# Kernel tuning notes

Measured on AMD Instinct MI355X. Metric: run time of the kernel, lower is better.

Reference implementation:

```python
import jax, jax.numpy as jnp
import numpy as np

D_MODEL = 2048
N_HEADS = 16
N_KV = 4
D_HEAD = D_MODEL // N_HEADS  # 128
N_REP = N_HEADS // N_KV      # 4
ROPE_BASE = 1000000.0


def _rope_tables(T, d_head, dtype):
    # inv_freq = (1/base)^(2i/d) for i in [0, d/2)
    i = jnp.arange(d_head // 2, dtype=jnp.float32)
    inv_freq = (1.0 / ROPE_BASE) ** (2.0 * i / d_head)
    theta = jnp.arange(T, dtype=jnp.float32)[:, None] * inv_freq[None, :]  # [T, d/2]
    theta = jnp.concatenate([theta, theta], axis=-1)                        # [T, d]
    return jnp.sin(theta).astype(dtype), jnp.cos(theta).astype(dtype)


def _apply_rope(x, sin, cos):
    # x: [B, h, T, d]; sin/cos: [T, d]
    x1, x2 = jnp.split(x, 2, axis=-1)
    rot = jnp.concatenate([-x2, x1], axis=-1)
    return cos[None, None] * x + sin[None, None] * rot


def setup_inputs() -> dict:
    key = jax.random.key(0)
    ks = jax.random.split(key, 9)
    B, T = 2, 2048
    s_in = 1.0 / np.sqrt(D_MODEL)
    return {
        "x": jax.random.normal(ks[0], (B, T, D_MODEL), jnp.float32),
        "wq": jax.random.normal(ks[1], (D_MODEL, N_HEADS * D_HEAD), jnp.float32) * s_in,
        "bq": jax.random.normal(ks[2], (N_HEADS * D_HEAD,), jnp.float32) * 0.02,
        "wk": jax.random.normal(ks[3], (D_MODEL, N_KV * D_HEAD), jnp.float32) * s_in,
        "bk": jax.random.normal(ks[4], (N_KV * D_HEAD,), jnp.float32) * 0.02,
        "wv": jax.random.normal(ks[5], (D_MODEL, N_KV * D_HEAD), jnp.float32) * s_in,
        "bv": jax.random.normal(ks[6], (N_KV * D_HEAD,), jnp.float32) * 0.02,
        "wo": jax.random.normal(ks[7], (D_MODEL, D_MODEL), jnp.float32) * s_in,
    }


def reference(x, wq, bq, wk, bk, wv, bv, wo):
    B, T, C = x.shape
    sin, cos = _rope_tables(T, D_HEAD, x.dtype)

    q = (x @ wq + bq).reshape(B, T, N_HEADS, D_HEAD).transpose(0, 2, 1, 3)  # [B,H,T,d]
    k = (x @ wk + bk).reshape(B, T, N_KV, D_HEAD).transpose(0, 2, 1, 3)     # [B,KV,T,d]
    v = (x @ wv + bv).reshape(B, T, N_KV, D_HEAD).transpose(0, 2, 1, 3)     # [B,KV,T,d]

    q = _apply_rope(q, sin, cos)
    k = _apply_rope(k, sin, cos)

    # GQA: group query heads as [B, KV, rep, T, d] to broadcast against k/v
    qg = q.reshape(B, N_KV, N_REP, T, D_HEAD)
    scale = 1.0 / jnp.sqrt(jnp.asarray(D_HEAD, x.dtype))
    scores = jnp.einsum('bkrqd,bksd->bkrqs', qg, k) * scale  # [B,KV,rep,T,S]

    causal = jnp.tril(jnp.ones((T, T), dtype=bool))
    neg = jnp.asarray(jnp.finfo(x.dtype).min, x.dtype)
    scores = jnp.where(causal[None, None, None], scores, neg)
    p = jax.nn.softmax(scores, axis=-1)

    out = jnp.einsum('bkrqs,bksd->bkrqd', p, v)               # [B,KV,rep,T,d]
    out = out.reshape(B, N_HEADS, T, D_HEAD).transpose(0, 2, 1, 3).reshape(B, T, C)
    return out @ wo, k, v
```

## Files before the change

kernel.cpp:

```cpp
#include <hip/hip_runtime.h>
#include <hip/hip_bf16.h>
#include <math.h>

#define BB 2
#define TT 2048
#define DMODEL 2048
#define NH 16
#define NKV 4
#define DH 128
#define NQKV 3072
#define MM (BB*TT)

typedef unsigned short u16;
typedef unsigned int u32;

typedef __bf16 bf16x8 __attribute__((ext_vector_type(8)));
typedef __bf16 bf16x4 __attribute__((ext_vector_type(4)));
typedef short short4v __attribute__((ext_vector_type(4)));
typedef float f32x4 __attribute__((ext_vector_type(4)));

__device__ __forceinline__ u16 f2b(float f) {
  union { float f; u32 u; } v; v.f = f;
  u32 r = v.u + 0x7fffu + ((v.u >> 16) & 1u);
  return (u16)(r >> 16);
}
__device__ __forceinline__ float b2f(u16 h) {
  union { u32 u; float f; } v; v.u = ((u32)h) << 16;
  return v.f;
}
__device__ __forceinline__ u32 pack2bf(float x, float y) {
  union { float f; u32 u; } a, b; a.f = x; b.f = y;
  return ((a.u + 0x8000u) >> 16) | ((b.u + 0x8000u) & 0xffff0000u);
}

__device__ __forceinline__ void gload16(const void* g, void* l) {
  __builtin_amdgcn_global_load_lds(
      (const __attribute__((address_space(1))) unsigned int*)g,
      (__attribute__((address_space(3))) unsigned int*)l, 16, 0, 0);
}

__device__ __forceinline__ float fast_exp2(float x) {
#if __has_builtin(__builtin_amdgcn_exp2f)
  return __builtin_amdgcn_exp2f(x);
#else
  return __expf(x * 0.6931471805599453f);
#endif
}

__device__ __forceinline__ f32x4 mfma16(bf16x4 a, bf16x4 b, f32x4 c) {
#if __has_builtin(__builtin_amdgcn_mfma_f32_16x16x16bf16_1k)
  union { bf16x4 b; short4v s; } ua, ub;
  ua.b = a; ub.b = b;
  return __builtin_amdgcn_mfma_f32_16x16x16bf16_1k(ua.s, ub.s, c, 0, 0, 0);
#elif __has_builtin(__builtin_amdgcn_mfma_f32_16x16x16_bf16)
  return __builtin_amdgcn_mfma_f32_16x16x16_bf16(a, b, c, 0, 0, 0);
#else
  asm volatile("v_mfma_f32_16x16x16_bf16 %0, %1, %2, %0"
               : "+v"(c) : "v"(a), "v"(b));
  return c;
#endif
}

__global__ void cvt_x_kernel(const float* __restrict__ x, u16* __restrict__ xb, int n4) {
  int i = blockIdx.x * 256 + threadIdx.x;
  if (i < n4) {
    float4 v = ((const float4*)x)[i];
    u32 lo = (u32)f2b(v.x) | ((u32)f2b(v.y) << 16);
    u32 hi = (u32)f2b(v.z) | ((u32)f2b(v.w) << 16);
    uint2 r; r.x = lo; r.y = hi;
    ((uint2*)xb)[i] = r;
  }
}

__global__ void rope_table_kernel(float2* __restrict__ tab) {
  int i = blockIdx.x * 256 + threadIdx.x;
  int t = i >> 6, d = i & 63;
  float inv = exp2f(-(float)d * 0.31143075889569023f);
  float th = (float)t * inv;
  float2 cs; cs.x = cosf(th); cs.y = sinf(th);
  tab[i] = cs;
}

__global__ void transpose_cvt_kernel(const float* __restrict__ src, u16* __restrict__ dst,
                                     int srcCols, int dstRowOff) {
  __shared__ u16 t[64][65];
  int c0 = blockIdx.x * 64, r0 = blockIdx.y * 64;
  int tid = threadIdx.x;
  for (int i = tid; i < 4096; i += 256) {
    int r = i >> 6, c = i & 63;
    t[r][c] = f2b(src[(size_t)(r0 + r) * srcCols + c0 + c]);
  }
  __syncthreads();
  for (int i = tid; i < 4096; i += 256) {
    int n = i >> 6, k = i & 63;
    dst[(size_t)(dstRowOff + c0 + n) * 2048 + r0 + k] = t[k][n];
  }
}

__global__ __launch_bounds__(256, 3) void gemm_qkv_kernel(
    const u16* __restrict__ A, const u16* __restrict__ Bt,
    const float* __restrict__ bq, const float* __restrict__ bk,
    const float* __restrict__ bv, const float2* __restrict__ rtab,
    u16* __restrict__ qb, u16* __restrict__ kb, u16* __restrict__ vt,
    float* __restrict__ outK, float* __restrict__ outV) {
  __shared__ __align__(16) u16 sm[16384];
  const int K = DMODEL;
  const int tid  = threadIdx.x;
  const int lane = tid & 63;
  const int wave = tid >> 6;
  const int quad = lane >> 4;
  const int l16  = lane & 15;
  const int m0 = blockIdx.y * 128;
  const int n0 = blockIdx.x * 128;
  const int nh = blockIdx.x;
  const int wrow = (wave >> 1) * 64;
  const int wcol = (wave & 1) * 64;

  f32x4 acc[4][4];
  const f32x4 zero = {0.f, 0.f, 0.f, 0.f};
#pragma unroll
  for (int i = 0; i < 4; i++)
#pragma unroll
    for (int j = 0; j < 4; j++) acc[i][j] = zero;

  const int srow = tid >> 2;
  const int scol = (tid & 3) * 8;
  const u16* ga = A  + (size_t)(m0 + srow) * K + scol;
  const u16* gb = Bt + (size_t)(n0 + srow) * K + scol;

  gload16(ga,                  &sm[tid * 8]);
  gload16(ga + (size_t)64 * K, &sm[2048 + tid * 8]);
  gload16(gb,                  &sm[4096 + tid * 8]);
  gload16(gb + (size_t)64 * K, &sm[6144 + tid * 8]);

  for (int k0 = 0; k0 < K; k0 += 32) {
    const int p = (k0 >> 5) & 1;
    const int kn = (k0 + 32 == K) ? 0 : k0 + 32;
    u16* nb = &sm[(p ^ 1) * 8192];
    gload16(ga + kn,                  nb + tid * 8);
    gload16(ga + kn + (size_t)64 * K, nb + 2048 + tid * 8);
    gload16(gb + kn,                  nb + 4096 + tid * 8);
    gload16(gb + kn + (size_t)64 * K, nb + 6144 + tid * 8);
    asm volatile("s_waitcnt vmcnt(4)\n\ts_barrier" ::: "memory");
    const u16* cb = &sm[p * 8192];
    bf16x8 af[4], bf[4];
#pragma unroll
    for (int mi = 0; mi < 4; mi++)
      af[mi] = *(const bf16x8*)&cb[(wrow + mi * 16 + l16) * 32 + quad * 8];
#pragma unroll
    for (int ni = 0; ni < 4; ni++)
      bf[ni] = *(const bf16x8*)&cb[4096 + (wcol + ni * 16 + l16) * 32 + quad * 8];
    asm volatile("s_waitcnt lgkmcnt(0)\n\ts_barrier" ::: "memory");
#pragma unroll
    for (int mi = 0; mi < 4; mi++)
#pragma unroll
      for (int ni = 0; ni < 4; ni++)
        acc[mi][ni] = __builtin_amdgcn_mfma_f32_16x16x32_bf16(af[mi], bf[ni], acc[mi][ni], 0, 0, 0);
  }

  asm volatile("s_waitcnt vmcnt(0)\n\ts_barrier" ::: "memory");

#pragma unroll
  for (int ni = 0; ni < 4; ni++) {
    int col = wcol + ni * 16 + l16;
    int gcol = n0 + col;
    float bval = (nh < 16) ? bq[gcol] : ((nh < 20) ? bk[gcol - 2048] : bv[gcol - 2560]);
#pragma unroll
    for (int mi = 0; mi < 4; mi++) {
#pragma unroll
      for (int r = 0; r < 4; r++) {
        int row = wrow + mi * 16 + quad * 4 + r;
        sm[row * 128 + col] = f2b(acc[mi][ni][r] + bval);
      }
    }
  }
  __syncthreads();

  const int bidx = m0 >> 11;
  const int trow0 = m0 & 2047;

  if (nh < 20) {
    const int isQ = (nh < 16);
    const int hh = isQ ? nh : (nh - 16);
#pragma unroll
    for (int it = 0; it < 4; it++) {
      int id = tid + it * 256;
      int row = id >> 3, oc = id & 7;
      int t = trow0 + row;
      int rl = t & 63, ttile = t >> 6;
      uint4 lo = *(const uint4*)&sm[row * 128 + oc * 8];
      uint4 hi = *(const uint4*)&sm[row * 128 + 64 + oc * 8];
      const u16* plo = (const u16*)&lo;
      const u16* phi = (const u16*)&hi;
      u16 y1[8], y2[8];
      float f1[8], f2v[8];
#pragma unroll
      for (int j = 0; j < 8; j++) {
        float2 cs = rtab[(t << 6) + oc * 8 + j];
        float x1 = b2f(plo[j]), x2 = b2f(phi[j]);
        f1[j]  = cs.x * x1 - cs.y * x2;
        f2v[j] = cs.x * x2 + cs.y * x1;
        y1[j] = f2b(f1[j]);
        y2[j] = f2b(f2v[j]);
      }
      if (isQ) {
        size_t tb = ((size_t)(bidx * NH + hh) * 32 + ttile) * 8192;
        *(uint4*)&qb[tb + (size_t)((oc)     * 64 + rl) * 8] = *(const uint4*)y1;
        *(uint4*)&qb[tb + (size_t)((oc + 8) * 64 + rl) * 8] = *(const uint4*)y2;
      } else {
        size_t tb = ((size_t)(bidx * NKV + hh) * 32 + ttile) * 8192;
        *(uint4*)&kb[tb + (size_t)((oc)     * 64 + rl) * 8] = *(const uint4*)y1;
        *(uint4*)&kb[tb + (size_t)((oc + 8) * 64 + rl) * 8] = *(const uint4*)y2;
        size_t base = ((size_t)(bidx * NKV + hh) * TT + t) * DH + oc * 8;
        *(float4*)&outK[base]          = *(const float4*)&f1[0];
        *(float4*)&outK[base + 4]      = *(const float4*)&f1[4];
        *(float4*)&outK[base + 64]     = *(const float4*)&f2v[0];
        *(float4*)&outK[base + 64 + 4] = *(const float4*)&f2v[4];
      }
    }
  } else {
    const int kvh = nh - 20;
#pragma unroll
    for (int it = 0; it < 8; it++) {
      int id = tid + it * 256;
      int row = id >> 4, oc = id & 15;
      uint4 v = *(const uint4*)&sm[row * 128 + oc * 8];
      const u16* pv = (const u16*)&v;
      float f[8];
#pragma unroll
      for (int j = 0; j < 8; j++) f[j] = b2f(pv[j]);
      size_t base = ((size_t)(bidx * NKV + kvh) * TT + trow0 + row) * DH + oc * 8;
      *(float4*)&outV[base]     = *(const float4*)&f[0];
      *(float4*)&outV[base + 4] = *(const float4*)&f[4];
    }
#pragma unroll
    for (int it = 0; it < 8; it++) {
      int id = tid + it * 256;
      int tile = id >> 10, rem = id & 1023;
      int chunk = rem >> 7, dl = rem & 127;
      int m = chunk >> 2, qd = chunk & 3;
      u16 tmp[8];
#pragma unroll
      for (int e = 0; e < 8; e++) {
        int srw = (2 * m + (e >> 2)) * 16 + qd * 4 + (e & 3);
        tmp[e] = sm[(tile * 64 + srw) * 128 + dl];
      }
      int tt = (trow0 >> 6) + tile;
      size_t tilebase = ((size_t)(bidx * NKV + kvh) * 32 + tt) * 8192;
      *(uint4*)&vt[tilebase + (size_t)(chunk * 128 + dl) * 8] = *(const uint4*)tmp;
    }
  }
}

__global__ __launch_bounds__(256, 3) void gemm_out_kernel(
    const u16* __restrict__ A, const u16* __restrict__ Bt,
    float* __restrict__ Cout, int M, int N, int K) {
  __shared__ __align__(16) u16 sm[16384];
  const int tid  = threadIdx.x;
  const int lane = tid & 63;
  const int wave = tid >> 6;
  const int quad = lane >> 4;
  const int l16  = lane & 15;
  const int m0 = blockIdx.y * 128;
  const int n0 = blockIdx.x * 128;
  const int wrow = (wave >> 1) * 64;
  const int wcol = (wave & 1) * 64;

  f32x4 acc[4][4];
  const f32x4 zero = {0.f, 0.f, 0.f, 0.f};
#pragma unroll
  for (int i = 0; i < 4; i++)
#pragma unroll
    for (int j = 0; j < 4; j++) acc[i][j] = zero;

  const int srow = tid >> 2;
  const int scol = (tid & 3) * 8;
  const u16* ga = A  + (size_t)(m0 + srow) * K + scol;
  const u16* gb = Bt + (size_t)(n0 + srow) * K + scol;

  gload16(ga,                  &sm[tid * 8]);
  gload16(ga + (size_t)64 * K, &sm[2048 + tid * 8]);
  gload16(gb,                  &sm[4096 + tid * 8]);
  gload16(gb + (size_t)64 * K, &sm[6144 + tid * 8]);

  for (int k0 = 0; k0 < K; k0 += 32) {
    const int p = (k0 >> 5) & 1;
    const int kn = (k0 + 32 == K) ? 0 : k0 + 32;
    u16* nb = &sm[(p ^ 1) * 8192];
    gload16(ga + kn,                  nb + tid * 8);
    gload16(ga + kn + (size_t)64 * K, nb + 2048 + tid * 8);
    gload16(gb + kn,                  nb + 4096 + tid * 8);
    gload16(gb + kn + (size_t)64 * K, nb + 6144 + tid * 8);
    asm volatile("s_waitcnt vmcnt(4)\n\ts_barrier" ::: "memory");
    const u16* cb = &sm[p * 8192];
    bf16x8 af[4], bf[4];
#pragma unroll
    for (int mi = 0; mi < 4; mi++)
      af[mi] = *(const bf16x8*)&cb[(wrow + mi * 16 + l16) * 32 + quad * 8];
#pragma unroll
    for (int ni = 0; ni < 4; ni++)
      bf[ni] = *(const bf16x8*)&cb[4096 + (wcol + ni * 16 + l16) * 32 + quad * 8];
    asm volatile("s_waitcnt lgkmcnt(0)\n\ts_barrier" ::: "memory");
#pragma unroll
    for (int mi = 0; mi < 4; mi++)
#pragma unroll
      for (int ni = 0; ni < 4; ni++)
        acc[mi][ni] = __builtin_amdgcn_mfma_f32_16x16x32_bf16(af[mi], bf[ni], acc[mi][ni], 0, 0, 0);
  }
  asm volatile("s_waitcnt vmcnt(0)" ::: "memory");

#pragma unroll
  for (int ni = 0; ni < 4; ni++) {
    int gcol = n0 + wcol + ni * 16 + l16;
#pragma unroll
    for (int mi = 0; mi < 4; mi++) {
#pragma unroll
      for (int r = 0; r < 4; r++) {
        int grow = m0 + wrow + mi * 16 + quad * 4 + r;
        Cout[(size_t)grow * N + gcol] = acc[mi][ni][r];
      }
    }
  }
}

__global__ __launch_bounds__(256, 2) void attn_kernel(
    const u16* __restrict__ Qt, const u16* __restrict__ Kt,
    const u16* __restrict__ Vt, u16* __restrict__ Ob) {
  __shared__ __align__(16) u16 sm[24576];
  u16* vbuf = sm + 16384;

  const int bh = blockIdx.y;
  const int b = bh >> 4, h = bh & 15, kv = h >> 2;
  const int tid = threadIdx.x;
  const int lane = tid & 63;
  const int wave = tid >> 6;
  const int quad = lane >> 4;
  const int l16 = lane & 15;

  const u16* qbase = Qt + (size_t)(b * NH + h) * 32 * 8192;
  const u16* kbase = Kt + (size_t)(b * NKV + kv) * 32 * 8192;
  const u16* vbase = Vt + (size_t)(b * NKV + kv) * 32 * 8192;

  const f32x4 zero = {0.f, 0.f, 0.f, 0.f};
  const float SC2 = 0.08838834764831845f * 1.4426950408889634f;
  const float NEGINF = -__builtin_inff();

  int par = 0;

#pragma unroll
  for (int p = 0; p < 4; p++)
    gload16(kbase + p * 2048 + tid * 8, sm + p * 2048 + tid * 8);

  for (int half = 0; half < 2; ++half) {
    const int qt = half ? (31 - (int)blockIdx.x) : (int)blockIdx.x;
    const int q0 = qt * 64;
    const u16* qtile = qbase + (size_t)qt * 8192;
    const int qrel = wave * 16 + l16;

    bf16x8 qf[4];
#pragma unroll
    for (int kc = 0; kc < 4; kc++)
      qf[kc] = *(const bf16x8*)&qtile[(size_t)((kc * 4 + quad) * 64 + qrel) * 8];

    float mrow = NEGINF, lrow = 0.f;
    f32x4 o[8];
#pragma unroll
    for (int d = 0; d < 8; d++) o[d] = zero;

    for (int kt = 0; kt <= qt; ++kt) {
      u16* kb_c = sm + par * 8192;
      u16* kb_n = sm + (par ^ 1) * 8192;
      const int ktn = (kt < qt) ? kt + 1 : 0;
      const u16* vsrc = vbase + (size_t)kt * 8192;
      const u16* knxt = kbase + (size_t)ktn * 8192;
#pragma unroll
      for (int p = 0; p < 4; p++)
        gload16(vsrc + p * 2048 + tid * 8, vbuf + p * 2048 + tid * 8);
#pragma unroll
      for (int p = 0; p < 4; p++)
        gload16(knxt + p * 2048 + tid * 8, kb_n + p * 2048 + tid * 8);
      asm volatile("s_waitcnt vmcnt(8)\n\ts_barrier" ::: "memory");

      f32x4 sv[4];
#pragma unroll
      for (int mt = 0; mt < 4; mt++) sv[mt] = zero;
#pragma unroll
      for (int kc = 0; kc < 4; kc++) {
#pragma unroll
        for (int mt = 0; mt < 4; mt++) {
          bf16x8 kf = *(const bf16x8*)&kb_c[(size_t)((kc * 4 + quad) * 64 + mt * 16 + l16) * 8];
          sv[mt] = __builtin_amdgcn_mfma_f32_16x16x32_bf16(kf, qf[kc], sv[mt], 0, 0, 0);
        }
      }

      if (kt == qt) {
#pragma unroll
        for (int mt = 0; mt < 4; mt++)
#pragma unroll
          for (int r = 0; r < 4; r++) {
            int srel = mt * 16 + quad * 4 + r;
            if (srel > qrel) sv[mt][r] = NEGINF;
          }
      }
      float mraw = NEGINF;
#pragma unroll
      for (int mt = 0; mt < 4; mt++)
#pragma unroll
        for (int r = 0; r < 4; r++) mraw = fmaxf(mraw, sv[mt][r]);
      mraw = fmaxf(mraw, __shfl_xor(mraw, 16));
      mraw = fmaxf(mraw, __shfl_xor(mraw, 32));

      float mnew = fmaxf(mrow, mraw);
      float alpha = fast_exp2((mrow - mnew) * SC2);
      mrow = mnew;
      float msc = mnew * SC2;
      float lsum = 0.f;
#pragma unroll
      for (int mt = 0; mt < 4; mt++) {
#pragma unroll
        for (int r = 0; r < 4; r++) {
          float p = fast_exp2(__builtin_fmaf(sv[mt][r], SC2, -msc));
          sv[mt][r] = p;
          lsum += p;
        }
      }
      lrow = lrow * alpha + lsum;
      bf16x4 pb[4];
#pragma unroll
      for (int mt = 0; mt < 4; mt++) {
        union { u32 u[2]; bf16x4 v; } pu;
        pu.u[0] = pack2bf(sv[mt][0], sv[mt][1]);
        pu.u[1] = pack2bf(sv[mt][2], sv[mt][3]);
        pb[mt] = pu.v;
      }
#pragma unroll
      for (int dt = 0; dt < 8; dt++) {
        o[dt][0] *= alpha; o[dt][1] *= alpha; o[dt][2] *= alpha; o[dt][3] *= alpha;
      }

      asm volatile("s_waitcnt vmcnt(4)\n\ts_barrier" ::: "memory");
#pragma unroll
      for (int m = 0; m < 2; m++) {
#pragma unroll
        for (int dt = 0; dt < 8; dt++) {
          bf16x8 vf = *(const bf16x8*)&vbuf[(size_t)(((m * 4 + quad) * 128) + dt * 16 + l16) * 8];
          bf16x4 vlo = __builtin_shufflevector(vf, vf, 0, 1, 2, 3);
          bf16x4 vhi = __builtin_shufflevector(vf, vf, 4, 5, 6, 7);
          o[dt] = mfma16(vlo, pb[2 * m],     o[dt]);
          o[dt] = mfma16(vhi, pb[2 * m + 1], o[dt]);
        }
      }
      asm volatile("s_barrier" ::: "memory");
      par ^= 1;
    }

    lrow += __shfl_xor(lrow, 16);
    lrow += __shfl_xor(lrow, 32);
    float inv = 1.0f / lrow;
    int t = q0 + qrel;
    size_t rowbase = (size_t)(b * TT + t) * DMODEL + h * DH;
#pragma unroll
    for (int dt = 0; dt < 8; dt++) {
      uint2 w;
      w.x = pack2bf(o[dt][0] * inv, o[dt][1] * inv);
      w.y = pack2bf(o[dt][2] * inv, o[dt][3] * inv);
      *(uint2*)&Ob[rowbase + dt * 16 + quad * 4] = w;
    }
  }
  asm volatile("s_waitcnt vmcnt(0)" ::: "memory");
}

extern "C" void kernel_launch(void* const* d_in, const int* in_sizes, int n_in,
                              void* d_out, int out_size, void* d_ws, size_t ws_size,
                              hipStream_t stream) {
  (void)in_sizes; (void)n_in; (void)out_size; (void)ws_size;
  const float* x  = (const float*)d_in[0];
  const float* wq = (const float*)d_in[1];
  const float* bq = (const float*)d_in[2];
  const float* wk = (const float*)d_in[3];
  const float* bk = (const float*)d_in[4];
  const float* wv = (const float*)d_in[5];
  const float* bv = (const float*)d_in[6];
  const float* wo = (const float*)d_in[7];
  float* out = (float*)d_out;

  char* ws = (char*)d_ws;
  u16*    xb    = (u16*)(ws);
  u16*    wqkvT = (u16*)(ws + 16777216);
  u16*    woT   = (u16*)(ws + 29360128);
  float2* rtab  = (float2*)(ws + 37748736);
  u16*    qb    = (u16*)(ws + 38797312);
  u16*    kb    = (u16*)(ws + 55574528);
  u16*    vt    = (u16*)(ws + 59768832);
  u16*    ob    = (u16*)(ws + 63963136);

  float* outK = out + (size_t)BB * TT * DMODEL;
  float* outV = outK + (size_t)BB * NKV * TT * DH;

  cvt_x_kernel<<<8192, 256, 0, stream>>>(x, xb, (BB * TT * DMODEL) / 4);
  rope_table_kernel<<<512, 256, 0, stream>>>(rtab);
  transpose_cvt_kernel<<<dim3(32, 32), 256, 0, stream>>>(wq, wqkvT, 2048, 0);
  transpose_cvt_kernel<<<dim3(8, 32),  256, 0, stream>>>(wk, wqkvT, 512, 2048);
  transpose_cvt_kernel<<<dim3(8, 32),  256, 0, stream>>>(wv, wqkvT, 512, 2560);
  transpose_cvt_kernel<<<dim3(32, 32), 256, 0, stream>>>(wo, woT, 2048, 0);

  gemm_qkv_kernel<<<dim3(NQKV / 128, MM / 128), 256, 0, stream>>>(
      xb, wqkvT, bq, bk, bv, rtab, qb, kb, vt, outK, outV);

  attn_kernel<<<dim3(16, BB * NH), 256, 0, stream>>>(qb, kb, vt, ob);

  gemm_out_kernel<<<dim3(DMODEL / 128, MM / 128), 256, 0, stream>>>(
      ob, woT, out, MM, DMODEL, DMODEL);
}
```

Before: 307.4 us.

## Rewrite QKV GEMM with 256x256 tiles, 8 waves, swizzled LDS and interleaved staging

The QKV projection GEMM moves from 128x128 tiles with 4 waves to 256x256 tiles with 8 waves. It uses a 128 KB double-buffered LDS layout with XOR swizzling, a K-step of 64, and a hand-scheduled four-phase loop. That loop interleaves global-to-LDS staging with MFMA quadrants and raises wave priority during the matrix ops. The aim is more data reuse per loaded byte, fewer LDS bank conflicts, and better overlap of memory and compute. In exchange the grid shrinks to 12x16 blocks, which may underfill the CUs, and the epilogue must handle two heads per block with swizzled indexing.

```diff
diff --git a/kernel.cpp b/kernel.cpp
--- a/kernel.cpp
+++ b/kernel.cpp
@@ -97,99 +97,173 @@
   }
 }
 
-__global__ __launch_bounds__(256, 3) void gemm_qkv_kernel(
+
+#define BARRIER asm volatile("s_barrier" ::: "memory")
+#define LGKM0   asm volatile("s_waitcnt lgkmcnt(0)" ::: "memory")
+
+#define STAGE_A(H, KT, RB) do { \
+    const u16* g_ = gA + (size_t)(H) * 262144 + (size_t)(KT) * 64; \
+    gload16(g_,          sm + (RB) + tid * 8); \
+    gload16(g_ + 131072, sm + (RB) + 4096 + tid * 8); \
+  } while (0)
+
+#define STAGE_B(H, KT, RB) do { \
+    const u16* g_ = gB + (size_t)(H) * 262144 + (size_t)(KT) * 64; \
+    gload16(g_,          sm + (RB) + tid * 8); \
+    gload16(g_ + 131072, sm + (RB) + 4096 + tid * 8); \
+  } while (0)
+
+#define LDA(BU, MH) do { \
+    const u16* ab_ = sm + (BU) + (MH) * 8192 + lra * 64; \
+    _Pragma("unroll") \
+    for (int mi = 0; mi < 4; mi++) { \
+      a[mi][0] = *(const bf16x8*)&ab_[mi * 1024 + as0]; \
+      a[mi][1] = *(const bf16x8*)&ab_[mi * 1024 + as1]; \
+    } \
+  } while (0)
+
+#define LDB(BU, NL) do { \
+    const u16* bb_ = sm + (BU) + 16384 + hb * 8192 + lrb * 64; \
+    _Pragma("unroll") \
+    for (int nj = 0; nj < 2; nj++) { \
+      b[(NL)*2+nj][0] = *(const bf16x8*)&bb_[((NL)*2+nj) * 1024 + bs0]; \
+      b[(NL)*2+nj][1] = *(const bf16x8*)&bb_[((NL)*2+nj) * 1024 + bs1]; \
+    } \
+  } while (0)
+
+#define MFMAQ(MH, NL) do { \
+    _Pragma("unroll") \
+    for (int mi = 0; mi < 4; mi++) \
+      _Pragma("unroll") \
+      for (int nj = 0; nj < 2; nj++) { \
+        acc[(MH)*4+mi][(NL)*2+nj] = __builtin_amdgcn_mfma_f32_16x16x32_bf16( \
+            a[mi][0], b[(NL)*2+nj][0], acc[(MH)*4+mi][(NL)*2+nj], 0, 0, 0); \
+        acc[(MH)*4+mi][(NL)*2+nj] = __builtin_amdgcn_mfma_f32_16x16x32_bf16( \
+            a[mi][1], b[(NL)*2+nj][1], acc[(MH)*4+mi][(NL)*2+nj], 0, 0, 0); \
+      } \
+  } while (0)
+
+#define TILE4(BU, OBU, KA1, KN) do { \
+     \
+    LDA(BU, 0); LDB(BU, 0); \
+    STAGE_A(1, KA1, (OBU) + 8192); \
+    BARRIER; LGKM0; \
+    __builtin_amdgcn_s_setprio(1); MFMAQ(0, 0); __builtin_amdgcn_s_setprio(0); \
+    BARRIER; \
+     \
+    LDB(BU, 1); \
+    STAGE_A(0, KN, (BU)); \
+    BARRIER; LGKM0; \
+    __builtin_amdgcn_s_setprio(1); MFMAQ(0, 1); __builtin_amdgcn_s_setprio(0); \
+    BARRIER; \
+     \
+    LDA(BU, 1); \
+    STAGE_B(0, KN, (BU) + 16384); \
+    BARRIER; LGKM0; \
+    __builtin_amdgcn_s_setprio(1); MFMAQ(1, 1); __builtin_amdgcn_s_setprio(0); \
+    BARRIER; \
+     \
+    STAGE_B(1, KN, (BU) + 24576); \
+    BARRIER; LGKM0; \
+    __builtin_amdgcn_s_setprio(1); MFMAQ(1, 0); __builtin_amdgcn_s_setprio(0); \
+    asm volatile("s_waitcnt vmcnt(6)\n\ts_barrier" ::: "memory"); \
+  } while (0)
+
+__global__ __launch_bounds__(512, 2) void gemm_qkv_kernel(
     const u16* __restrict__ A, const u16* __restrict__ Bt,
     const float* __restrict__ bq, const float* __restrict__ bk,
     const float* __restrict__ bv, const float2* __restrict__ rtab,
     u16* __restrict__ qb, u16* __restrict__ kb, u16* __restrict__ vt,
     float* __restrict__ outK, float* __restrict__ outV) {
-  __shared__ __align__(16) u16 sm[16384];
-  const int K = DMODEL;
+  __shared__ __align__(16) u16 sm[65536];
   const int tid  = threadIdx.x;
   const int lane = tid & 63;
   const int wave = tid >> 6;
+  const int wm   = wave >> 2;
+  const int wn   = wave & 3;
   const int quad = lane >> 4;
   const int l16  = lane & 15;
-  const int m0 = blockIdx.y * 128;
-  const int n0 = blockIdx.x * 128;
-  const int nh = blockIdx.x;
-  const int wrow = (wave >> 1) * 64;
-  const int wcol = (wave & 1) * 64;
-
-  f32x4 acc[4][4];
+  const int m0 = blockIdx.y * 256;
+  const int n0 = blockIdx.x * 256;
+  const int bx = blockIdx.x;
+
+  const int srow = tid >> 3;
+  const int sch  = (tid & 7) ^ (srow & 7);
+  const u16* gA = A  + (size_t)(m0 + srow) * 2048 + sch * 8;
+  const u16* gB = Bt + (size_t)(n0 + srow) * 2048 + sch * 8;
+
+  const int lra = wm * 64 + l16;
+  const int lrb = (wn & 1) * 64 + l16;
+  const int hb  = wn >> 1;
+  const int as0 = ((quad)     ^ (lra & 7)) << 3;
+  const int as1 = ((quad + 4) ^ (lra & 7)) << 3;
+  const int bs0 = ((quad)     ^ (lrb & 7)) << 3;
+  const int bs1 = ((quad + 4) ^ (lrb & 7)) << 3;
+
+  bf16x8 a[4][2], b[4][2];
+  f32x4 acc[8][4];
   const f32x4 zero = {0.f, 0.f, 0.f, 0.f};
 #pragma unroll
-  for (int i = 0; i < 4; i++)
+  for (int i = 0; i < 8; i++)
 #pragma unroll
     for (int j = 0; j < 4; j++) acc[i][j] = zero;
 
-  const int srow = tid >> 2;
-  const int scol = (tid & 3) * 8;
-  const u16* ga = A  + (size_t)(m0 + srow) * K + scol;
-  const u16* gb = Bt + (size_t)(n0 + srow) * K + scol;
-
-  gload16(ga,                  &sm[tid * 8]);
-  gload16(ga + (size_t)64 * K, &sm[2048 + tid * 8]);
-  gload16(gb,                  &sm[4096 + tid * 8]);
-  gload16(gb + (size_t)64 * K, &sm[6144 + tid * 8]);
-
-  for (int k0 = 0; k0 < K; k0 += 32) {
-    const int p = (k0 >> 5) & 1;
-    const int kn = (k0 + 32 == K) ? 0 : k0 + 32;
-    u16* nb = &sm[(p ^ 1) * 8192];
-    gload16(ga + kn,                  nb + tid * 8);
-    gload16(ga + kn + (size_t)64 * K, nb + 2048 + tid * 8);
-    gload16(gb + kn,                  nb + 4096 + tid * 8);
-    gload16(gb + kn + (size_t)64 * K, nb + 6144 + tid * 8);
-    asm volatile("s_waitcnt vmcnt(4)\n\ts_barrier" ::: "memory");
-    const u16* cb = &sm[p * 8192];
-    bf16x8 af[4], bf[4];
-#pragma unroll
-    for (int mi = 0; mi < 4; mi++)
-      af[mi] = *(const bf16x8*)&cb[(wrow + mi * 16 + l16) * 32 + quad * 8];
-#pragma unroll
-    for (int ni = 0; ni < 4; ni++)
-      bf[ni] = *(const bf16x8*)&cb[4096 + (wcol + ni * 16 + l16) * 32 + quad * 8];
-    asm volatile("s_waitcnt lgkmcnt(0)\n\ts_barrier" ::: "memory");
-#pragma unroll
-    for (int mi = 0; mi < 4; mi++)
-#pragma unroll
-      for (int ni = 0; ni < 4; ni++)
-        acc[mi][ni] = __builtin_amdgcn_mfma_f32_16x16x32_bf16(af[mi], bf[ni], acc[mi][ni], 0, 0, 0);
+  STAGE_A(0, 0, 0);
+  STAGE_B(0, 0, 16384);
+  STAGE_B(1, 0, 24576);
+  STAGE_A(1, 0, 8192);
+  STAGE_A(0, 1, 32768);
+  STAGE_B(0, 1, 32768 + 16384);
+  STAGE_B(1, 1, 32768 + 24576);
+  asm volatile("s_waitcnt vmcnt(6)\n\ts_barrier" ::: "memory");
+
+#pragma unroll 1
+  for (int it2 = 0; it2 < 16; ++it2) {
+    const int ka1 = (2 * it2 + 1) & 31;
+    const int kn0 = (2 * it2 + 2) & 31;
+    const int kn1 = (2 * it2 + 3) & 31;
+    TILE4(0,     32768, ka1, kn0);
+    TILE4(32768, 0,     kn0, kn1);
   }
 
   asm volatile("s_waitcnt vmcnt(0)\n\ts_barrier" ::: "memory");
 
-#pragma unroll
-  for (int ni = 0; ni < 4; ni++) {
-    int col = wcol + ni * 16 + l16;
+  const int cls = (bx < 8) ? 0 : ((bx < 10) ? 1 : 2);
+#pragma unroll
+  for (int nf = 0; nf < 4; nf++) {
+    int col = wn * 64 + nf * 16 + l16;
     int gcol = n0 + col;
-    float bval = (nh < 16) ? bq[gcol] : ((nh < 20) ? bk[gcol - 2048] : bv[gcol - 2560]);
-#pragma unroll
-    for (int mi = 0; mi < 4; mi++) {
-#pragma unroll
-      for (int r = 0; r < 4; r++) {
-        int row = wrow + mi * 16 + quad * 4 + r;
-        sm[row * 128 + col] = f2b(acc[mi][ni][r] + bval);
-      }
-    }
+    float bval = (cls == 0) ? bq[gcol] : ((cls == 1) ? bk[gcol - 2048] : bv[gcol - 2560]);
+#pragma unroll
+    for (int mh = 0; mh < 2; mh++)
+#pragma unroll
+      for (int mi = 0; mi < 4; mi++)
+#pragma unroll
+        for (int r = 0; r < 4; r++) {
+          int row = mh * 128 + wm * 64 + mi * 16 + quad * 4 + r;
+          int ci = (row * 256 + col) ^ ((row & 7) << 3);
+          sm[ci] = f2b(acc[mh * 4 + mi][nf][r] + bval);
+        }
   }
   __syncthreads();
 
   const int bidx = m0 >> 11;
   const int trow0 = m0 & 2047;
 
-  if (nh < 20) {
-    const int isQ = (nh < 16);
-    const int hh = isQ ? nh : (nh - 16);
-#pragma unroll
-    for (int it = 0; it < 4; it++) {
-      int id = tid + it * 256;
-      int row = id >> 3, oc = id & 7;
+  if (cls < 2) {
+    const int isQ = (cls == 0);
+#pragma unroll
+    for (int itq = 0; itq < 8; itq++) {
+      int id = tid + itq * 512;
+      int lh = id >> 11;
+      int rem = id & 2047;
+      int row = rem >> 3, oc = rem & 7;
       int t = trow0 + row;
       int rl = t & 63, ttile = t >> 6;
-      uint4 lo = *(const uint4*)&sm[row * 128 + oc * 8];
-      uint4 hi = *(const uint4*)&sm[row * 128 + 64 + oc * 8];
+      int sw = (row & 7) << 3;
+      int i0 = (row * 256 + lh * 128 + oc * 8);
+      uint4 lo = *(const uint4*)&sm[i0 ^ sw];
+      uint4 hi = *(const uint4*)&sm[(i0 + 64) ^ sw];
       const u16* plo = (const u16*)&lo;
       const u16* phi = (const u16*)&hi;
       u16 y1[8], y2[8];
@@ -204,10 +278,12 @@
         y2[j] = f2b(f2v[j]);
       }
       if (isQ) {
+        int hh = bx * 2 + lh;
         size_t tb = ((size_t)(bidx * NH + hh) * 32 + ttile) * 8192;
         *(uint4*)&qb[tb + (size_t)((oc)     * 64 + rl) * 8] = *(const uint4*)y1;
         *(uint4*)&qb[tb + (size_t)((oc + 8) * 64 + rl) * 8] = *(const uint4*)y2;
       } else {
+        int hh = bx * 2 + lh - 16;
         size_t tb = ((size_t)(bidx * NKV + hh) * 32 + ttile) * 8192;
         *(uint4*)&kb[tb + (size_t)((oc)     * 64 + rl) * 8] = *(const uint4*)y1;
         *(uint4*)&kb[tb + (size_t)((oc + 8) * 64 + rl) * 8] = *(const uint4*)y2;
@@ -219,12 +295,15 @@
       }
     }
   } else {
-    const int kvh = nh - 20;
-#pragma unroll
-    for (int it = 0; it < 8; it++) {
-      int id = tid + it * 256;
-      int row = id >> 4, oc = id & 15;
-      uint4 v = *(const uint4*)&sm[row * 128 + oc * 8];
+#pragma unroll
+    for (int itv = 0; itv < 16; itv++) {
+      int id = tid + itv * 512;
+      int lh = id >> 12;
+      int rem = id & 4095;
+      int row = rem >> 4, oc = rem & 15;
+      int kvh = bx * 2 + lh - 20;
+      int i0 = (row * 256 + lh * 128 + oc * 8) ^ ((row & 7) << 3);
+      uint4 v = *(const uint4*)&sm[i0];
       const u16* pv = (const u16*)&v;
       float f[8];
 #pragma unroll
@@ -234,18 +313,24 @@
       *(float4*)&outV[base + 4] = *(const float4*)&f[4];
     }
 #pragma unroll
-    for (int it = 0; it < 8; it++) {
-      int id = tid + it * 256;
-      int tile = id >> 10, rem = id & 1023;
-      int chunk = rem >> 7, dl = rem & 127;
+    for (int itv = 0; itv < 16; itv++) {
+      int id = tid + itv * 512;
+      int lh = id >> 12;
+      int rem = id & 4095;
+      int st = rem >> 10;
+      int rem2 = rem & 1023;
+      int chunk = rem2 >> 7, dl = rem2 & 127;
       int m = chunk >> 2, qd = chunk & 3;
+      int kvh = bx * 2 + lh - 20;
       u16 tmp[8];
 #pragma unroll
       for (int e = 0; e < 8; e++) {
         int srw = (2 * m + (e >> 2)) * 16 + qd * 4 + (e & 3);
-        tmp[e] = sm[(tile * 64 + srw) * 128 + dl];
-      }
-      int tt = (trow0 >> 6) + tile;
+        int row = st * 64 + srw;
+        int idx = (row * 256 + lh * 128 + dl) ^ ((row & 7) << 3);
+        tmp[e] = sm[idx];
+      }
+      int tt = (trow0 >> 6) + st;
       size_t tilebase = ((size_t)(bidx * NKV + kvh) * 32 + tt) * 8192;
       *(uint4*)&vt[tilebase + (size_t)(chunk * 128 + dl) * 8] = *(const uint4*)tmp;
     }
@@ -255,7 +340,7 @@
 __global__ __launch_bounds__(256, 3) void gemm_out_kernel(
     const u16* __restrict__ A, const u16* __restrict__ Bt,
     float* __restrict__ Cout, int M, int N, int K) {
-  __shared__ __align__(16) u16 sm[16384];
+  __shared__ __align__(16) u16 smo[16384];
   const int tid  = threadIdx.x;
   const int lane = tid & 63;
   const int wave = tid >> 6;
@@ -278,21 +363,21 @@
   const u16* ga = A  + (size_t)(m0 + srow) * K + scol;
   const u16* gb = Bt + (size_t)(n0 + srow) * K + scol;
 
-  gload16(ga,                  &sm[tid * 8]);
-  gload16(ga + (size_t)64 * K, &sm[2048 + tid * 8]);
-  gload16(gb,                  &sm[4096 + tid * 8]);
-  gload16(gb + (size_t)64 * K, &sm[6144 + tid * 8]);
+  gload16(ga,                  &smo[tid * 8]);
+  gload16(ga + (size_t)64 * K, &smo[2048 + tid * 8]);
+  gload16(gb,                  &smo[4096 + tid * 8]);
+  gload16(gb + (size_t)64 * K, &smo[6144 + tid * 8]);
 
   for (int k0 = 0; k0 < K; k0 += 32) {
     const int p = (k0 >> 5) & 1;
     const int kn = (k0 + 32 == K) ? 0 : k0 + 32;
-    u16* nb = &sm[(p ^ 1) * 8192];
+    u16* nb = &smo[(p ^ 1) * 8192];
     gload16(ga + kn,                  nb + tid * 8);
     gload16(ga + kn + (size_t)64 * K, nb + 2048 + tid * 8);
     gload16(gb + kn,                  nb + 4096 + tid * 8);
     gload16(gb + kn + (size_t)64 * K, nb + 6144 + tid * 8);
     asm volatile("s_waitcnt vmcnt(4)\n\ts_barrier" ::: "memory");
-    const u16* cb = &sm[p * 8192];
+    const u16* cb = &smo[p * 8192];
     bf16x8 af[4], bf[4];
 #pragma unroll
     for (int mi = 0; mi < 4; mi++)
@@ -504,7 +589,7 @@
   transpose_cvt_kernel<<<dim3(8, 32),  256, 0, stream>>>(wv, wqkvT, 512, 2560);
   transpose_cvt_kernel<<<dim3(32, 32), 256, 0, stream>>>(wo, woT, 2048, 0);
 
-  gemm_qkv_kernel<<<dim3(NQKV / 128, MM / 128), 256, 0, stream>>>(
+  gemm_qkv_kernel<<<dim3(NQKV / 256, MM / 256), 512, 0, stream>>>(
       xb, wqkvT, bq, bk, bv, rtab, qb, kb, vt, outK, outV);
 
   attn_kernel<<<dim3(16, BB * NH), 256, 0, stream>>>(qb, kb, vt, ob);
```

New measurement: 303.3 us. Within noise of the previous version (-1.3%).
